# Kernel tuning notes

Hardware: AMD Instinct MI355X
Metric: run time of the kernel (lower is better)

The kernel has to match this reference:

```python
import jax, jax.numpy as jnp
import numpy as np
from itertools import product

DIM = 384
HEADS = 8
DIM_HEAD = 64
INNER = HEADS * DIM_HEAD  # 512
KS = 3                    # kernel_size (attention window)
PAD = KS // 2
W_WIN = KS * KS           # 9
SCALE = DIM_HEAD ** -0.5


def setup_inputs() -> dict:
    key = jax.random.key(0)
    k1, k2, k3, k4, k5 = jax.random.split(key, 5)
    B, H, W = 4, 56, 56
    x = jax.random.normal(k1, (B, DIM, H, W), dtype=jnp.float32)
    # 1x1 conv weights stored as (out_ch, in_ch)
    Wq = jax.random.normal(k2, (INNER, DIM), dtype=jnp.float32) * (DIM ** -0.5)
    Wkv = jax.random.normal(k3, (2 * INNER, DIM), dtype=jnp.float32) * (DIM ** -0.5)
    Wo = jax.random.normal(k4, (DIM, INNER), dtype=jnp.float32) * (INNER ** -0.5)
    bo = jax.random.normal(k5, (DIM,), dtype=jnp.float32) * 0.01
    return {"x": x, "Wq": Wq, "Wkv": Wkv, "Wo": Wo, "bo": bo}


def _conv1x1(x, w):
    # x: (B,Cin,H,W), w: (Cout,Cin) -> (B,Cout,H,W)
    return jnp.einsum('bchw,oc->bohw', x, w)


def reference(x, Wq, Wkv, Wo, bo):
    B, C, H, W = x.shape
    q = _conv1x1(x, Wq)                       # (B, INNER, H, W)
    kv = _conv1x1(x, Wkv)                     # (B, 2*INNER, H, W)
    k, v = jnp.split(kv, 2, axis=1)
    # split channels heads-major, matching torch reshape (B, heads, dh, H, W)
    q = q.reshape(B, HEADS, DIM_HEAD, H, W)
    k = k.reshape(B, HEADS, DIM_HEAD, H, W)
    v = v.reshape(B, HEADS, DIM_HEAD, H, W)
    # zero-pad spatial dims (matches F.unfold zero padding: padded taps get logit 0)
    k_pad = jnp.pad(k, ((0, 0), (0, 0), (0, 0), (PAD, PAD), (PAD, PAD)))
    v_pad = jnp.pad(v, ((0, 0), (0, 0), (0, 0), (PAD, PAD), (PAD, PAD)))
    offsets = list(product(range(KS), range(KS)))  # row-major = unfold order
    # dots: (B, heads, H, W, w)
    dots = jnp.stack([
        jnp.einsum('bhdxy,bhdxy->bhxy', q, k_pad[:, :, :, i:i + H, j:j + W])
        for (i, j) in offsets
    ], axis=-1) * SCALE
    attn = jax.nn.softmax(dots, axis=-1)      # softmax over the 9-tap window
    # weighted sum of shifted v: (B, heads, dh, H, W)
    out = sum(
        attn[:, :, None, :, :, w_idx] * v_pad[:, :, :, i:i + H, j:j + W]
        for w_idx, (i, j) in enumerate(offsets)
    )
    out = out.reshape(B, INNER, H, W)
    return _conv1x1(out, Wo) + bo[None, :, None, None]
```

## Files before the change

kernel.cpp:

```cpp
#include <hip/hip_runtime.h>


#define HW 3136
#define WIMG 56
#define QKV_CH 1536
#define SCALE 0.125f
#define SLEN 200

typedef __bf16 bf16x8_t __attribute__((ext_vector_type(8)));
typedef float f32x4_t __attribute__((ext_vector_type(4)));

__device__ __forceinline__ float bf2f(unsigned short u) {
    return __uint_as_float(((unsigned int)u) << 16);
}
__device__ __forceinline__ unsigned short f2bf(float f) {
    unsigned int u = __float_as_uint(f);
    u += 0x7FFFu + ((u >> 16) & 1u);
    return (unsigned short)(u >> 16);
}
__device__ __forceinline__ int gpos(int g, int row) { return (g + ((row >> 1) & 3)) & 3; }

__global__ __launch_bounds__(256) void cvt_bf16(
    const float* __restrict__ in, unsigned short* __restrict__ out, int n4)
{
    const int i = blockIdx.x * 256 + threadIdx.x;
    if (i >= n4) return;
    const float4 v = reinterpret_cast<const float4*>(in)[i];
    uint2 u;
    u.x = (unsigned int)f2bf(v.x) | ((unsigned int)f2bf(v.y) << 16);
    u.y = (unsigned int)f2bf(v.z) | ((unsigned int)f2bf(v.w) << 16);
    reinterpret_cast<uint2*>(out)[i] = u;
}

template <int K, bool OUT_F32>
__global__ __launch_bounds__(256) void gemm_mfma(
    const unsigned short* __restrict__ Xb,
    const unsigned short* __restrict__ Wb,
    const float* __restrict__ bias,
    unsigned short* __restrict__ out_bf,
    float* __restrict__ out_f,
    int M)
{
    __shared__ __align__(16) unsigned short A_lds[128 * 32];
    __shared__ __align__(16) unsigned short B_lds[64 * 32];

    const int s0 = blockIdx.x * 64;
    const int o0 = blockIdx.y * 128;
    const int b  = blockIdx.z;
    const int t  = threadIdx.x;
    const int lane = t & 63, w = t >> 6;
    const int quad = lane >> 4, mrow = lane & 15;

    const int ar = t >> 2, ag = t & 3;
    const int bs = t & 63, bg = t >> 6;

    const unsigned short* xp = Xb + (size_t)b * K * HW + s0 + bs;
    const unsigned short* wr0 = Wb + (size_t)(o0 + ar) * K;
    const unsigned short* wr1 = Wb + (size_t)(o0 + 64 + ar) * K;

    f32x4_t acc[2][4];
#pragma unroll
    for (int m = 0; m < 2; m++)
#pragma unroll
        for (int nt = 0; nt < 4; nt++) acc[m][nt] = (f32x4_t){0.f, 0.f, 0.f, 0.f};

    for (int k0 = 0; k0 < K; k0 += 32) {
        const uint4 a0 = *reinterpret_cast<const uint4*>(wr0 + k0 + ag * 8);
        const uint4 a1 = *reinterpret_cast<const uint4*>(wr1 + k0 + ag * 8);
        __align__(16) unsigned short bv[8];
#pragma unroll
        for (int j = 0; j < 8; j++)
            bv[j] = xp[(size_t)(k0 + bg * 8 + j) * HW];

        __syncthreads();
        *reinterpret_cast<uint4*>(&A_lds[ar * 32 + gpos(ag, ar) * 8]) = a0;
        *reinterpret_cast<uint4*>(&A_lds[(64 + ar) * 32 + gpos(ag, 64 + ar) * 8]) = a1;
        *reinterpret_cast<uint4*>(&B_lds[bs * 32 + gpos(bg, bs) * 8]) =
            *reinterpret_cast<const uint4*>(bv);
        __syncthreads();

        bf16x8_t bfr[4];
#pragma unroll
        for (int nt = 0; nt < 4; nt++) {
            const int srow = nt * 16 + mrow;
            bfr[nt] = *reinterpret_cast<const bf16x8_t*>(&B_lds[srow * 32 + gpos(quad, srow) * 8]);
        }
#pragma unroll
        for (int m = 0; m < 2; m++) {
            const int orow = w * 32 + m * 16 + mrow;
            const bf16x8_t af = *reinterpret_cast<const bf16x8_t*>(&A_lds[orow * 32 + gpos(quad, orow) * 8]);
#pragma unroll
            for (int nt = 0; nt < 4; nt++)
                acc[m][nt] = __builtin_amdgcn_mfma_f32_16x16x32_bf16(af, bfr[nt], acc[m][nt], 0, 0, 0);
        }
    }

#pragma unroll
    for (int m = 0; m < 2; m++)
#pragma unroll
        for (int nt = 0; nt < 4; nt++)
#pragma unroll
            for (int r = 0; r < 4; r++) {
                const int oo = o0 + w * 32 + m * 16 + quad * 4 + r;
                const int ss = s0 + nt * 16 + mrow;
                if (OUT_F32) {
                    out_f[(size_t)b * M * HW + (size_t)oo * HW + ss] = acc[m][nt][r] + bias[oo];
                } else {
                    out_bf[(size_t)b * M * HW + (size_t)oo * HW + ss] = f2bf(acc[m][nt][r]);
                }
            }
}

__global__ __launch_bounds__(256) void natt2(
    const unsigned short* __restrict__ qkv,
    unsigned short* __restrict__ ao)
{
    __shared__ __align__(16) unsigned short smem[2 * 64 * SLEN];
    unsigned short* Kl = smem;
    unsigned short* Vl = smem + 64 * SLEN;
    float* dred = reinterpret_cast<float*>(smem);

    const int t = threadIdx.x, lane = t & 63, w = t >> 6;
    const int s0 = blockIdx.x * 64;
    const int s  = s0 + lane;
    const int h  = blockIdx.y, b = blockIdx.z;
    const int y  = s / WIMG, xx = s % WIMG;

    const size_t hbase = (size_t)b * QKV_CH * HW + (size_t)(h * 64) * HW;
    const unsigned short* kg = qkv + hbase + (size_t)512 * HW;
    const unsigned short* vg = qkv + hbase + (size_t)1024 * HW;

#pragma unroll
    for (int i = 0; i < 6; i++) {
        const int f = i * 256 + t;
        const int d = f / 24, j = f % 24;
        int g = s0 - 64 + j * 8;
        g = min(max(g, 0), HW - 8);
        const uint4 k4 = *reinterpret_cast<const uint4*>(kg + (size_t)d * HW + g);
        const uint4 v4 = *reinterpret_cast<const uint4*>(vg + (size_t)d * HW + g);
        *reinterpret_cast<uint4*>(&Kl[d * SLEN + j * 8]) = k4;
        *reinterpret_cast<uint4*>(&Vl[d * SLEN + j * 8]) = v4;
    }

    int   off9[9];
    float msk[9];
#pragma unroll
    for (int ty = 0; ty < 3; ty++)
#pragma unroll
        for (int tx = 0; tx < 3; tx++) {
            const int tap = ty * 3 + tx;
            const int ny = y + ty - 1, nx = xx + tx - 1;
            const bool v = (ny >= 0) && (ny < WIMG) && (nx >= 0) && (nx < WIMG);
            off9[tap] = v ? ((ty - 1) * WIMG + (tx - 1)) : 0;
            msk[tap]  = v ? 1.f : 0.f;
        }

    __syncthreads();

    const unsigned short* qp = qkv + hbase + s;
    float dots[9];
#pragma unroll
    for (int tp = 0; tp < 9; tp++) dots[tp] = 0.f;
#pragma unroll 4
    for (int dd = 0; dd < 16; dd++) {
        const int d = w * 16 + dd;
        const float qv = bf2f(qp[(size_t)d * HW]);
        const int bi = d * SLEN + lane + 64;
#pragma unroll
        for (int tp = 0; tp < 9; tp++)
            dots[tp] += qv * bf2f(Kl[bi + off9[tp]]);
    }

    __syncthreads();
#pragma unroll
    for (int tp = 0; tp < 9; tp++) dred[(tp * 4 + w) * 64 + lane] = dots[tp];
    __syncthreads();

    float mx = -1e30f, dt[9];
#pragma unroll
    for (int tp = 0; tp < 9; tp++) {
        const float sum = dred[(tp * 4 + 0) * 64 + lane] + dred[(tp * 4 + 1) * 64 + lane] +
                          dred[(tp * 4 + 2) * 64 + lane] + dred[(tp * 4 + 3) * 64 + lane];
        dt[tp] = msk[tp] * (sum * SCALE);
        mx = fmaxf(mx, dt[tp]);
    }
    float se = 0.f, w9[9];
#pragma unroll
    for (int tp = 0; tp < 9; tp++) { w9[tp] = __expf(dt[tp] - mx); se += w9[tp]; }
    const float inv = 1.f / se;
#pragma unroll
    for (int tp = 0; tp < 9; tp++) w9[tp] *= inv * msk[tp];

    unsigned short* aop = ao + (size_t)b * 512 * HW + (size_t)(h * 64) * HW + s;
#pragma unroll 4
    for (int dd = 0; dd < 16; dd++) {
        const int d = w * 16 + dd;
        const int bi = d * SLEN + lane + 64;
        float o = 0.f;
#pragma unroll
        for (int tp = 0; tp < 9; tp++)
            o += w9[tp] * bf2f(Vl[bi + off9[tp]]);
        aop[(size_t)d * HW] = f2bf(o);
    }
}

extern "C" void kernel_launch(void* const* d_in, const int* in_sizes, int n_in,
                              void* d_out, int out_size, void* d_ws, size_t ws_size,
                              hipStream_t stream) {
    const float* x   = (const float*)d_in[0];
    const float* Wq  = (const float*)d_in[1];
    const float* Wkv = (const float*)d_in[2];
    const float* Wo  = (const float*)d_in[3];
    const float* bo  = (const float*)d_in[4];
    float* out = (float*)d_out;

    unsigned short* xb   = (unsigned short*)d_ws;
    unsigned short* wb   = xb + (size_t)4 * 384 * HW;
    unsigned short* wob  = wb + (size_t)1536 * 384;
    unsigned short* qkvb = wob + (size_t)384 * 512;
    unsigned short* aob  = qkvb + (size_t)4 * QKV_CH * HW;

    cvt_bf16<<<dim3(4704), 256, 0, stream>>>(x, xb, 1204224);
    cvt_bf16<<<dim3(192),  256, 0, stream>>>(Wq, wb, 49152);
    cvt_bf16<<<dim3(384),  256, 0, stream>>>(Wkv, wb + 196608, 98304);
    cvt_bf16<<<dim3(192),  256, 0, stream>>>(Wo, wob, 49152);

    gemm_mfma<384, false><<<dim3(49, 12, 4), 256, 0, stream>>>(
        xb, wb, nullptr, qkvb, nullptr, QKV_CH);
    natt2<<<dim3(49, 8, 4), 256, 0, stream>>>(qkvb, aob);
    gemm_mfma<512, true><<<dim3(49, 3, 4), 256, 0, stream>>>(
        aob, wob, bo, nullptr, out, 384);
}
```

Measured before the change: 157.9 us.

## Pre-tile x into transposed bf16 blocks and stream them into LDS directly

The x conversion kernel now also transposes x into per-(spatial block, k block) tiles laid out spatial-major. This lets the QKV GEMM fetch its B operand with one contiguous 16-byte global_load_lds per thread instead of eight strided 2-byte loads. The three weight conversions are merged into one launch, and the generic GEMM template is split into two specialised kernels. The cost is an LDS transpose with scalar 2-byte stores in the conversion kernel, and the B tile in LDS now has no swizzle, which may cause bank conflicts.

```diff
diff --git a/kernel.cpp b/kernel.cpp
--- a/kernel.cpp
+++ b/kernel.cpp
@@ -20,26 +20,123 @@
 }
 __device__ __forceinline__ int gpos(int g, int row) { return (g + ((row >> 1) & 3)) & 3; }
 
-__global__ __launch_bounds__(256) void cvt_bf16(
-    const float* __restrict__ in, unsigned short* __restrict__ out, int n4)
+__global__ __launch_bounds__(256) void cvt_w_all(
+    const float* __restrict__ Wq, const float* __restrict__ Wkv,
+    const float* __restrict__ Wo, unsigned short* __restrict__ wdst)
 {
     const int i = blockIdx.x * 256 + threadIdx.x;
-    if (i >= n4) return;
-    const float4 v = reinterpret_cast<const float4*>(in)[i];
+    const float* src; int base;
+    if (i < 49152)       { src = Wq;  base = 0; }
+    else if (i < 147456) { src = Wkv; base = 49152; }
+    else                 { src = Wo;  base = 147456; }
+    const float4 v = reinterpret_cast<const float4*>(src)[i - base];
     uint2 u;
     u.x = (unsigned int)f2bf(v.x) | ((unsigned int)f2bf(v.y) << 16);
     u.y = (unsigned int)f2bf(v.z) | ((unsigned int)f2bf(v.w) << 16);
-    reinterpret_cast<uint2*>(out)[i] = u;
-}
-
-template <int K, bool OUT_F32>
-__global__ __launch_bounds__(256) void gemm_mfma(
-    const unsigned short* __restrict__ Xb,
+    reinterpret_cast<uint2*>(wdst)[i] = u;
+}
+
+__global__ __launch_bounds__(256) void cvtT_x(
+    const float* __restrict__ x, unsigned short* __restrict__ xT)
+{
+    __shared__ unsigned short Tl[64 * 36];
+    const int sblk = blockIdx.x, kblk = blockIdx.y, b = blockIdx.z;
+    const int t = threadIdx.x;
+
+    const float* xp = x + ((size_t)b * 384 + (size_t)kblk * 32) * HW + sblk * 64;
+    const int c = t >> 3;
+#pragma unroll
+    for (int i = 0; i < 2; i++) {
+        const int sc = (t & 7) + 8 * i;
+        const float4 v = *reinterpret_cast<const float4*>(xp + (size_t)c * HW + sc * 4);
+        const int s4 = sc * 4;
+        Tl[(s4 + 0) * 36 + c] = f2bf(v.x);
+        Tl[(s4 + 1) * 36 + c] = f2bf(v.y);
+        Tl[(s4 + 2) * 36 + c] = f2bf(v.z);
+        Tl[(s4 + 3) * 36 + c] = f2bf(v.w);
+    }
+    __syncthreads();
+
+    const int row = t >> 2, gran = t & 3;
+    const uint2 lo = *reinterpret_cast<const uint2*>(&Tl[row * 36 + gran * 8]);
+    const uint2 hi = *reinterpret_cast<const uint2*>(&Tl[row * 36 + gran * 8 + 4]);
+    uint4 o; o.x = lo.x; o.y = lo.y; o.z = hi.x; o.w = hi.y;
+    unsigned short* dst = xT + ((((size_t)b * 49 + sblk) * 12 + kblk) << 11);
+    *reinterpret_cast<uint4*>(dst + t * 8) = o;
+}
+
+__global__ __launch_bounds__(256) void gemm1(
+    const unsigned short* __restrict__ xT,
+    const unsigned short* __restrict__ Wb,
+    unsigned short* __restrict__ qkv)
+{
+    __shared__ __align__(16) unsigned short A_lds[128 * 32];
+    __shared__ __align__(16) unsigned short B_lds[64 * 32];
+
+    const int sblk = blockIdx.x;
+    const int o0 = blockIdx.y * 128;
+    const int b  = blockIdx.z;
+    const int t  = threadIdx.x;
+    const int lane = t & 63, w = t >> 6;
+    const int quad = lane >> 4, mrow = lane & 15;
+
+    const int ar = t >> 2, ag = t & 3;
+    const unsigned short* wr0 = Wb + (size_t)(o0 + ar) * 384;
+    const unsigned short* wr1 = Wb + (size_t)(o0 + 64 + ar) * 384;
+    const unsigned short* xsrc = xT + (((size_t)b * 49 + sblk) * 12 << 11)
+                               + w * 512 + lane * 8;
+
+    f32x4_t acc[2][4];
+#pragma unroll
+    for (int m = 0; m < 2; m++)
+#pragma unroll
+        for (int nt = 0; nt < 4; nt++) acc[m][nt] = (f32x4_t){0.f, 0.f, 0.f, 0.f};
+
+    for (int kb = 0; kb < 12; kb++) {
+        const uint4 a0 = *reinterpret_cast<const uint4*>(wr0 + kb * 32 + ag * 8);
+        const uint4 a1 = *reinterpret_cast<const uint4*>(wr1 + kb * 32 + ag * 8);
+
+        __syncthreads();
+        __builtin_amdgcn_global_load_lds(
+            (const __attribute__((address_space(1))) unsigned int*)(xsrc + (size_t)kb * 2048),
+            (__attribute__((address_space(3))) unsigned int*)(B_lds + w * 512),
+            16, 0, 0);
+        *reinterpret_cast<uint4*>(&A_lds[ar * 32 + gpos(ag, ar) * 8]) = a0;
+        *reinterpret_cast<uint4*>(&A_lds[(64 + ar) * 32 + gpos(ag, 64 + ar) * 8]) = a1;
+        __syncthreads();
+
+        bf16x8_t bfr[4];
+#pragma unroll
+        for (int nt = 0; nt < 4; nt++)
+            bfr[nt] = *reinterpret_cast<const bf16x8_t*>(&B_lds[(nt * 16 + mrow) * 32 + quad * 8]);
+#pragma unroll
+        for (int m = 0; m < 2; m++) {
+            const int orow = w * 32 + m * 16 + mrow;
+            const bf16x8_t af = *reinterpret_cast<const bf16x8_t*>(&A_lds[orow * 32 + gpos(quad, orow) * 8]);
+#pragma unroll
+            for (int nt = 0; nt < 4; nt++)
+                acc[m][nt] = __builtin_amdgcn_mfma_f32_16x16x32_bf16(af, bfr[nt], acc[m][nt], 0, 0, 0);
+        }
+    }
+
+    const int s0 = sblk * 64;
+#pragma unroll
+    for (int m = 0; m < 2; m++)
+#pragma unroll
+        for (int nt = 0; nt < 4; nt++)
+#pragma unroll
+            for (int r = 0; r < 4; r++) {
+                const int oo = o0 + w * 32 + m * 16 + quad * 4 + r;
+                const int ss = s0 + nt * 16 + mrow;
+                qkv[(size_t)b * QKV_CH * HW + (size_t)oo * HW + ss] = f2bf(acc[m][nt][r]);
+            }
+}
+
+__global__ __launch_bounds__(256) void gemm3(
+    const unsigned short* __restrict__ ao,
     const unsigned short* __restrict__ Wb,
     const float* __restrict__ bias,
-    unsigned short* __restrict__ out_bf,
-    float* __restrict__ out_f,
-    int M)
+    float* __restrict__ out)
 {
     __shared__ __align__(16) unsigned short A_lds[128 * 32];
     __shared__ __align__(16) unsigned short B_lds[64 * 32];
@@ -54,9 +151,9 @@
     const int ar = t >> 2, ag = t & 3;
     const int bs = t & 63, bg = t >> 6;
 
-    const unsigned short* xp = Xb + (size_t)b * K * HW + s0 + bs;
-    const unsigned short* wr0 = Wb + (size_t)(o0 + ar) * K;
-    const unsigned short* wr1 = Wb + (size_t)(o0 + 64 + ar) * K;
+    const unsigned short* xp = ao + (size_t)b * 512 * HW + s0 + bs;
+    const unsigned short* wr0 = Wb + (size_t)(o0 + ar) * 512;
+    const unsigned short* wr1 = Wb + (size_t)(o0 + 64 + ar) * 512;
 
     f32x4_t acc[2][4];
 #pragma unroll
@@ -64,7 +161,7 @@
 #pragma unroll
         for (int nt = 0; nt < 4; nt++) acc[m][nt] = (f32x4_t){0.f, 0.f, 0.f, 0.f};
 
-    for (int k0 = 0; k0 < K; k0 += 32) {
+    for (int k0 = 0; k0 < 512; k0 += 32) {
         const uint4 a0 = *reinterpret_cast<const uint4*>(wr0 + k0 + ag * 8);
         const uint4 a1 = *reinterpret_cast<const uint4*>(wr1 + k0 + ag * 8);
         __align__(16) unsigned short bv[8];
@@ -103,11 +200,7 @@
             for (int r = 0; r < 4; r++) {
                 const int oo = o0 + w * 32 + m * 16 + quad * 4 + r;
                 const int ss = s0 + nt * 16 + mrow;
-                if (OUT_F32) {
-                    out_f[(size_t)b * M * HW + (size_t)oo * HW + ss] = acc[m][nt][r] + bias[oo];
-                } else {
-                    out_bf[(size_t)b * M * HW + (size_t)oo * HW + ss] = f2bf(acc[m][nt][r]);
-                }
+                out[(size_t)b * 384 * HW + (size_t)oo * HW + ss] = acc[m][nt][r] + bias[oo];
             }
 }
 
@@ -214,20 +307,16 @@
     const float* bo  = (const float*)d_in[4];
     float* out = (float*)d_out;
 
-    unsigned short* xb   = (unsigned short*)d_ws;
-    unsigned short* wb   = xb + (size_t)4 * 384 * HW;
+    unsigned short* xT   = (unsigned short*)d_ws;
+    unsigned short* wb   = xT + (size_t)4 * 384 * HW;
     unsigned short* wob  = wb + (size_t)1536 * 384;
     unsigned short* qkvb = wob + (size_t)384 * 512;
     unsigned short* aob  = qkvb + (size_t)4 * QKV_CH * HW;
 
-    cvt_bf16<<<dim3(4704), 256, 0, stream>>>(x, xb, 1204224);
-    cvt_bf16<<<dim3(192),  256, 0, stream>>>(Wq, wb, 49152);
-    cvt_bf16<<<dim3(384),  256, 0, stream>>>(Wkv, wb + 196608, 98304);
-    cvt_bf16<<<dim3(192),  256, 0, stream>>>(Wo, wob, 49152);
-
-    gemm_mfma<384, false><<<dim3(49, 12, 4), 256, 0, stream>>>(
-        xb, wb, nullptr, qkvb, nullptr, QKV_CH);
+    cvt_w_all<<<dim3(768), 256, 0, stream>>>(Wq, Wkv, Wo, wb);
+    cvtT_x<<<dim3(49, 12, 4), 256, 0, stream>>>(x, xT);
+
+    gemm1<<<dim3(49, 12, 4), 256, 0, stream>>>(xT, wb, qkvb);
     natt2<<<dim3(49, 8, 4), 256, 0, stream>>>(qkvb, aob);
-    gemm_mfma<512, true><<<dim3(49, 3, 4), 256, 0, stream>>>(
-        aob, wob, bo, nullptr, out, 384);
-}
+    gemm3<<<dim3(49, 3, 4), 256, 0, stream>>>(aob, wob, bo, out);
+}
```

Measured after the change: 152.1 us. 1.04x faster.
